# Kernel tuning notes

Hardware: AMD Instinct MI355X
Metric: run time of the kernel (lower is better)

The kernel has to match this reference:

```python
import jax, jax.numpy as jnp
import numpy as np
import math

N_EMBED = 2048
N_HEAD = 16
HEAD_DIM = N_EMBED // N_HEAD  # 128
ROPE_BASE = 10000.0


def _rope_tables(T, dim, dtype):
    # inv_freq over even indices, emb = concat(freqs, freqs) along last dim
    inv_freq = 1.0 / (ROPE_BASE ** (jnp.arange(0, dim, 2, dtype=jnp.float32) / dim))
    t = jnp.arange(T, dtype=jnp.float32)
    freqs = jnp.einsum('i,j->ij', t, inv_freq)          # [T, dim/2]
    emb = jnp.concatenate([freqs, freqs], axis=-1)      # [T, dim]
    return jnp.cos(emb).astype(dtype), jnp.sin(emb).astype(dtype)


def _rotate_half(x):
    h = x.shape[-1] // 2
    return jnp.concatenate([-x[..., h:], x[..., :h]], axis=-1)


def setup_inputs() -> dict:
    key = jax.random.key(0)
    ks = jax.random.split(key, 5)
    B, T, C = 32, 256, N_EMBED
    s = 1.0 / math.sqrt(C)
    return {
        'x': jax.random.normal(ks[0], (B, T, C), dtype=jnp.float32),
        'wq': jax.random.normal(ks[1], (C, C), dtype=jnp.float32) * s,
        'wk': jax.random.normal(ks[2], (C, C), dtype=jnp.float32) * s,
        'wv': jax.random.normal(ks[3], (C, C), dtype=jnp.float32) * s,
        'wo': jax.random.normal(ks[4], (C, C), dtype=jnp.float32) * s,
    }


def reference(x, wq, wk, wv, wo):
    B, T, C = x.shape
    H, D = N_HEAD, HEAD_DIM
    # torch Linear: y = x @ W^T
    q = (x @ wq.T).reshape(B, T, H, D).transpose(0, 2, 1, 3)  # [B,H,T,D]
    k = (x @ wk.T).reshape(B, T, H, D).transpose(0, 2, 1, 3)
    v = (x @ wv.T).reshape(B, T, H, D).transpose(0, 2, 1, 3)

    cos, sin = _rope_tables(T, D, x.dtype)  # [T,D] each, broadcast over B,H
    q = q * cos + _rotate_half(q) * sin
    k = k * cos + _rotate_half(k) * sin

    att = jnp.einsum('bhqd,bhkd->bhqk', q, k) / math.sqrt(D)
    causal = jnp.triu(jnp.ones((T, T), dtype=bool), k=1)
    att = jnp.where(causal, jnp.finfo(att.dtype).min, att)
    att = jax.nn.softmax(att, axis=-1)
    # dropout p=0.0 -> identity
    y = jnp.einsum('bhqk,bhkd->bhqd', att, v)
    y = y.transpose(0, 2, 1, 3).reshape(B, T, C)
    return y @ wo.T
```

## Files before the change

kernel.cpp:

```cpp
#include <hip/hip_runtime.h>

#define HB 32
#define HT 256
#define HC 2048
#define HH 16
#define HD 128
#define HM (HB * HT)

typedef __bf16 bf16x8 __attribute__((ext_vector_type(8)));
typedef float f32x4 __attribute__((ext_vector_type(4)));

__device__ __forceinline__ unsigned short f2bf(float f) {
  unsigned u = __float_as_uint(f);
  u += 0x7FFFu + ((u >> 16) & 1u);
  return (unsigned short)(u >> 16);
}

__global__ __launch_bounds__(256) void cvt_all(
    const float* __restrict__ x, const float* __restrict__ wq, const float* __restrict__ wk,
    const float* __restrict__ wv, const float* __restrict__ wo,
    unsigned short* __restrict__ xb, unsigned short* __restrict__ wqb,
    unsigned short* __restrict__ wkb, unsigned short* __restrict__ wvb,
    unsigned short* __restrict__ wob) {
  size_t i = (size_t)blockIdx.x * 256 + threadIdx.x;
  const float* src;
  unsigned short* dst;
  size_t off;
  if (i < 4194304) {
    src = x; dst = xb; off = i;
  } else {
    size_t j = i - 4194304;
    int w = (int)(j >> 20);
    off = j & 1048575;
    src = (w == 0) ? wq : (w == 1) ? wk : (w == 2) ? wv : wo;
    dst = (w == 0) ? wqb : (w == 1) ? wkb : (w == 2) ? wvb : wob;
  }
  float4 v = ((const float4*)src)[off];
  ushort4 o;
  o.x = f2bf(v.x); o.y = f2bf(v.y); o.z = f2bf(v.z); o.w = f2bf(v.w);
  ((ushort4*)dst)[off] = o;
}

__device__ __forceinline__ void gl_lds16(const unsigned short* g, unsigned short* l) {
  __builtin_amdgcn_global_load_lds((const __attribute__((address_space(1))) void*)g,
                                   (__attribute__((address_space(3))) void*)l, 16, 0, 0);
}

__device__ __forceinline__ void gemm_core_wide(const unsigned short* __restrict__ Ab,
                                               const unsigned short* __restrict__ Wb,
                                               unsigned short* lsA, unsigned short* lsB,
                                               f32x4 acc[4][8], int tid) {
  const int lane = tid & 63, wave = tid >> 6;
  const int l16 = lane & 15, quad = lane >> 4;
  const int wr = wave >> 1, wc = wave & 1;
  const int ch = (quad ^ ((l16 >> 1) & 3)) * 8;

  for (int kt = 0; kt < HC / 64; ++kt) {
    __syncthreads();
#pragma unroll
    for (int i = 0; i < 4; i++) {
      int c = i * 256 + tid;
      int vrow = c >> 2, slot = c & 3;
      int gc = slot ^ ((vrow >> 1) & 3);
      int row = vrow & 127, kh = vrow >> 7;
      gl_lds16(Ab + (size_t)row * HC + kt * 64 + kh * 32 + gc * 8, lsA + c * 8);
    }
#pragma unroll
    for (int i = 0; i < 8; i++) {
      int c = i * 256 + tid;
      int vrow = c >> 2, slot = c & 3;
      int gc = slot ^ ((vrow >> 1) & 3);
      int row = vrow & 255, kh = vrow >> 8;
      gl_lds16(Wb + (size_t)row * HC + kt * 64 + kh * 32 + gc * 8, lsB + c * 8);
    }
    __syncthreads();
#pragma unroll
    for (int kh = 0; kh < 2; ++kh) {
      bf16x8 af[4], bfr[8];
#pragma unroll
      for (int mi = 0; mi < 4; mi++) {
        int r = wr * 64 + mi * 16 + l16;
        af[mi] = *(const bf16x8*)(lsA + (kh * 128 + r) * 32 + ch);
      }
#pragma unroll
      for (int nj = 0; nj < 8; nj++) {
        int r = wc * 128 + nj * 16 + l16;
        bfr[nj] = *(const bf16x8*)(lsB + (kh * 256 + r) * 32 + ch);
      }
#pragma unroll
      for (int mi = 0; mi < 4; mi++)
#pragma unroll
        for (int nj = 0; nj < 8; nj++)
          acc[mi][nj] = __builtin_amdgcn_mfma_f32_16x16x32_bf16(af[mi], bfr[nj], acc[mi][nj], 0, 0, 0);
    }
  }
}

__global__ __launch_bounds__(256, 2) void gemm_out(const unsigned short* __restrict__ A,
                                                   const unsigned short* __restrict__ W,
                                                   float* __restrict__ outp) {
  __shared__ __align__(16) unsigned short lsA[2 * 128 * 32];
  __shared__ __align__(16) unsigned short lsB[2 * 256 * 32];
  const int tid = threadIdx.x;
  const int lane = tid & 63, wave = tid >> 6;
  const int l16 = lane & 15, quad = lane >> 4;
  const int wr = wave >> 1, wc = wave & 1;
  const int bm = blockIdx.x, bn = blockIdx.y;

  f32x4 acc[4][8];
#pragma unroll
  for (int i = 0; i < 4; i++)
#pragma unroll
    for (int j = 0; j < 8; j++) acc[i][j] = f32x4{0.f, 0.f, 0.f, 0.f};

  gemm_core_wide(A + (size_t)bm * 128 * HC, W + (size_t)bn * 256 * HC, lsA, lsB, acc, tid);

#pragma unroll
  for (int mi = 0; mi < 4; mi++)
#pragma unroll
    for (int nj = 0; nj < 8; nj++) {
      const int n = bn * 256 + wc * 128 + nj * 16 + l16;
#pragma unroll
      for (int rr = 0; rr < 4; rr++) {
        const int m = bm * 128 + wr * 64 + mi * 16 + quad * 4 + rr;
        outp[(size_t)m * HC + n] = acc[mi][nj][rr];
      }
    }
}

__global__ __launch_bounds__(256, 2) void gemm_qkv(const unsigned short* __restrict__ A,
                                                    const unsigned short* __restrict__ W0,
                                                    const unsigned short* __restrict__ W1,
                                                    const unsigned short* __restrict__ W2,
                                                    unsigned short* __restrict__ Qo,
                                                    unsigned short* __restrict__ Ko,
                                                    unsigned short* __restrict__ Vto) {
  __shared__ __align__(16) unsigned short lsA[2 * 128 * 32];
  __shared__ __align__(16) unsigned short lsB[2 * 256 * 32];
  const int tid = threadIdx.x;
  const int lane = tid & 63, wave = tid >> 6;
  const int l16 = lane & 15, quad = lane >> 4;
  const int wr = wave >> 1, wc = wave & 1;
  const int bm = blockIdx.x;
  const int which = blockIdx.y >> 3;
  const int bn = blockIdx.y & 7;

  f32x4 acc[4][8];
#pragma unroll
  for (int i = 0; i < 4; i++)
#pragma unroll
    for (int j = 0; j < 8; j++) acc[i][j] = f32x4{0.f, 0.f, 0.f, 0.f};

  if (which < 2) {
    const unsigned short* W = (which == 0) ? W0 : W1;
    unsigned short* outp = (which == 0) ? Qo : Ko;
    gemm_core_wide(A + (size_t)bm * 128 * HC, W + (size_t)bn * 256 * HC, lsA, lsB, acc, tid);
    const int h = bn * 2 + wc;
#pragma unroll
    for (int nj = 0; nj < 4; nj++) {
      const int dlo = nj * 16 + l16;
      const float invf = __expf((float)dlo * (-0.14391156831212787f));
#pragma unroll
      for (int mi = 0; mi < 4; mi++)
#pragma unroll
        for (int rr = 0; rr < 4; rr++) {
          const int m = bm * 128 + wr * 64 + mi * 16 + quad * 4 + rr;
          const int t = m & 255, b = m >> 8;
          float ang = (float)t * invf;
          float sn, cs;
          __sincosf(ang, &sn, &cs);
          float lo = acc[mi][nj][rr], hi = acc[mi][nj + 4][rr];
          size_t base = (((size_t)b * HH + h) * HT + t) * HD;
          outp[base + dlo] = f2bf(lo * cs - hi * sn);
          outp[base + 64 + dlo] = f2bf(hi * cs + lo * sn);
        }
    }
  } else {
    int v = bn * 64 + bm;
    int tok = v & 31, ch2 = v >> 5;
    gemm_core_wide(W2 + (size_t)ch2 * 128 * HC, A + (size_t)tok * 256 * HC, lsA, lsB, acc, tid);
    const int b = tok, h = ch2;
#pragma unroll
    for (int mi = 0; mi < 4; mi++)
#pragma unroll
      for (int nj = 0; nj < 8; nj++) {
        const int t = wc * 128 + nj * 16 + l16;
#pragma unroll
        for (int rr = 0; rr < 4; rr++) {
          const int d = wr * 64 + mi * 16 + quad * 4 + rr;
          Vto[(((size_t)b * HH + h) * HD + d) * HT + t] = f2bf(acc[mi][nj][rr]);
        }
      }
  }
}

__global__ __launch_bounds__(256) void attn_kernel(const unsigned short* __restrict__ Q,
                                                   const unsigned short* __restrict__ K,
                                                   const unsigned short* __restrict__ Vt,
                                                   unsigned short* __restrict__ Y) {
  const int g = blockIdx.x;
  const int bh = g & 511;
  const int pairp = g >> 9;
  const int wave = threadIdx.x >> 6;
  const int lane = threadIdx.x & 63;
  const int quad = lane >> 4, l16 = lane & 15;

  const unsigned short* Qh = Q + (size_t)bh * HT * HD;
  const unsigned short* Kh = K + (size_t)bh * HT * HD;
  const unsigned short* Vh = Vt + (size_t)bh * HD * HT;

  __shared__ __align__(16) unsigned short P[4][16 * 72];
  unsigned short* Pw = P[wave];

  const float scale = 0.088388347648318447f;
  const int b = bh >> 4, h = bh & 15;

  for (int half = 0; half < 2; ++half) {
    const int wq = (pairp == 0) ? (half == 0 ? 3 : 0) : (half == 0 ? 2 : 1);
    const int qrow = wq * 64 + wave * 16;

    bf16x8 qf[4];
#pragma unroll
    for (int ks = 0; ks < 4; ks++)
      qf[ks] = *(const bf16x8*)(Qh + (size_t)(qrow + l16) * HD + ks * 32 + quad * 8);

    f32x4 o[8];
#pragma unroll
    for (int di = 0; di < 8; di++) o[di] = f32x4{0.f, 0.f, 0.f, 0.f};
    float mrow[4], lrow[4];
#pragma unroll
    for (int r = 0; r < 4; r++) { mrow[r] = -1e30f; lrow[r] = 0.f; }

    for (int ct = 0; ct <= wq; ++ct) {
      f32x4 s[4];
#pragma unroll
      for (int ni = 0; ni < 4; ni++) s[ni] = f32x4{0.f, 0.f, 0.f, 0.f};
      const int nimax = (ct == wq) ? wave : 3;
#pragma unroll
      for (int ksh = 0; ksh < 2; ksh++) {
        bf16x8 kf[4][2];
#pragma unroll
        for (int ni = 0; ni < 4; ni++)
          if (ni <= nimax)
#pragma unroll
            for (int k2 = 0; k2 < 2; k2++)
              kf[ni][k2] = *(const bf16x8*)(Kh + (size_t)(ct * 64 + ni * 16 + l16) * HD +
                                            (ksh * 2 + k2) * 32 + quad * 8);
#pragma unroll
        for (int k2 = 0; k2 < 2; k2++)
#pragma unroll
          for (int ni = 0; ni < 4; ni++)
            if (ni <= nimax)
              s[ni] = __builtin_amdgcn_mfma_f32_16x16x32_bf16(qf[ksh * 2 + k2], kf[ni][k2],
                                                              s[ni], 0, 0, 0);
      }
      bf16x8 vf0[8];
#pragma unroll
      for (int di = 0; di < 8; di++)
        vf0[di] = *(const bf16x8*)(Vh + (size_t)(di * 16 + l16) * HT + ct * 64 + quad * 8);

      if (ct == wq) {
#pragma unroll
        for (int ni = 0; ni < 4; ni++)
#pragma unroll
          for (int r = 0; r < 4; r++) {
            int qr = wave * 16 + quad * 4 + r;
            int kc = ni * 16 + l16;
            s[ni][r] = (kc <= qr) ? s[ni][r] * scale : -1e30f;
          }
      } else {
#pragma unroll
        for (int ni = 0; ni < 4; ni++)
#pragma unroll
          for (int r = 0; r < 4; r++) s[ni][r] *= scale;
      }
      float pm[4];
#pragma unroll
      for (int r = 0; r < 4; r++) {
        float v = fmaxf(fmaxf(s[0][r], s[1][r]), fmaxf(s[2][r], s[3][r]));
        v = fmaxf(v, __shfl_xor(v, 1, 64));
        v = fmaxf(v, __shfl_xor(v, 2, 64));
        v = fmaxf(v, __shfl_xor(v, 4, 64));
        v = fmaxf(v, __shfl_xor(v, 8, 64));
        pm[r] = v;
      }
      float ex = fmaxf(fmaxf(pm[0] - mrow[0], pm[1] - mrow[1]),
                       fmaxf(pm[2] - mrow[2], pm[3] - mrow[3]));
      ex = fmaxf(ex, __shfl_xor(ex, 16, 64));
      ex = fmaxf(ex, __shfl_xor(ex, 32, 64));
      if (ex > 8.f) {
#pragma unroll
        for (int r = 0; r < 4; r++) {
          float mnew = fmaxf(mrow[r], pm[r]);
          float alpha = __expf(mrow[r] - mnew);
          mrow[r] = mnew;
          lrow[r] *= alpha;
#pragma unroll
          for (int di = 0; di < 8; di++) o[di][r] *= alpha;
        }
      }
#pragma unroll
      for (int r = 0; r < 4; r++) {
        float rs = 0.f;
#pragma unroll
        for (int ni = 0; ni < 4; ni++) {
          float e = __expf(s[ni][r] - mrow[r]);
          s[ni][r] = e;
          rs += e;
        }
        rs += __shfl_xor(rs, 1, 64);
        rs += __shfl_xor(rs, 2, 64);
        rs += __shfl_xor(rs, 4, 64);
        rs += __shfl_xor(rs, 8, 64);
        lrow[r] += rs;
      }
#pragma unroll
      for (int ni = 0; ni < 4; ni++)
#pragma unroll
        for (int r = 0; r < 4; r++)
          Pw[(quad * 4 + r) * 72 + ni * 16 + l16] = f2bf(s[ni][r]);
      {
        bf16x8 pf = *(const bf16x8*)(Pw + (size_t)l16 * 72 + quad * 8);
#pragma unroll
        for (int di = 0; di < 8; di++)
          o[di] = __builtin_amdgcn_mfma_f32_16x16x32_bf16(pf, vf0[di], o[di], 0, 0, 0);
      }
      {
        bf16x8 pf = *(const bf16x8*)(Pw + (size_t)l16 * 72 + 32 + quad * 8);
#pragma unroll
        for (int di = 0; di < 8; di++) {
          bf16x8 vf = *(const bf16x8*)(Vh + (size_t)(di * 16 + l16) * HT + ct * 64 + 32 + quad * 8);
          o[di] = __builtin_amdgcn_mfma_f32_16x16x32_bf16(pf, vf, o[di], 0, 0, 0);
        }
      }
    }

#pragma unroll
    for (int r = 0; r < 4; r++) {
      float inv = 1.f / lrow[r];
      int t = qrow + quad * 4 + r;
      size_t rowb = ((size_t)b * HT + t) * HC + h * HD;
#pragma unroll
      for (int di = 0; di < 8; di++)
        Y[rowb + di * 16 + l16] = f2bf(o[di][r] * inv);
    }
  }
}

extern "C" void kernel_launch(void* const* d_in, const int* in_sizes, int n_in,
                              void* d_out, int out_size, void* d_ws, size_t ws_size,
                              hipStream_t stream) {
  const float* x  = (const float*)d_in[0];
  const float* wq = (const float*)d_in[1];
  const float* wk = (const float*)d_in[2];
  const float* wv = (const float*)d_in[3];
  const float* wo = (const float*)d_in[4];
  float* out = (float*)d_out;

  char* ws = (char*)d_ws;
  const size_t MB = (size_t)1 << 20;
  unsigned short* wqb = (unsigned short*)(ws + 0 * MB);
  unsigned short* wkb = (unsigned short*)(ws + 8 * MB);
  unsigned short* wvb = (unsigned short*)(ws + 16 * MB);
  unsigned short* wob = (unsigned short*)(ws + 24 * MB);
  unsigned short* xb  = (unsigned short*)(ws + 32 * MB);
  unsigned short* Qb  = (unsigned short*)(ws + 64 * MB);
  unsigned short* Kb  = (unsigned short*)(ws + 96 * MB);
  unsigned short* Vtb = (unsigned short*)(ws + 128 * MB);
  unsigned short* Yb  = xb;

  cvt_all<<<32768, 256, 0, stream>>>(x, wq, wk, wv, wo, xb, wqb, wkb, wvb, wob);

  gemm_qkv<<<dim3(HM / 128, 24), 256, 0, stream>>>(xb, wqb, wkb, wvb, Qb, Kb, Vtb);

  attn_kernel<<<1024, 256, 0, stream>>>(Qb, Kb, Vtb, Yb);

  gemm_out<<<dim3(HM / 128, HC / 256), 256, 0, stream>>>(Yb, wob, out);
}
```

Before: 498.4 us.

## Load GEMM A fragments directly from global into registers with prefetch

```diff
diff --git a/kernel.cpp b/kernel.cpp
--- a/kernel.cpp
+++ b/kernel.cpp
@@ -46,60 +46,71 @@
                                    (__attribute__((address_space(3))) void*)l, 16, 0, 0);
 }
 
-__device__ __forceinline__ void gemm_core_wide(const unsigned short* __restrict__ Ab,
+__device__ __forceinline__ void gemm_step(const unsigned short* __restrict__ Arow,
+                                          const unsigned short* __restrict__ Wb,
+                                          unsigned short* lsB, f32x4 acc[4][8],
+                                          bf16x8 afu[2][4], bf16x8 afp[2][4],
+                                          int kt, int ktp, int tid, int ch, int wc, int l16) {
+  __syncthreads();
+#pragma unroll
+  for (int i = 0; i < 8; i++) {
+    int c = i * 256 + tid;
+    int vrow = c >> 2, slot = c & 3;
+    int gc = slot ^ ((vrow >> 1) & 3);
+    int row = vrow & 255, kh = vrow >> 8;
+    gl_lds16(Wb + (size_t)row * HC + kt * 64 + kh * 32 + gc * 8, lsB + c * 8);
+  }
+  __syncthreads();
+  if (ktp >= 0) {
+#pragma unroll
+    for (int kh = 0; kh < 2; kh++)
+#pragma unroll
+      for (int mi = 0; mi < 4; mi++)
+        afp[kh][mi] = *(const bf16x8*)(Arow + (size_t)mi * (16 * HC) + ktp * 64 + kh * 32);
+  }
+#pragma unroll
+  for (int kh = 0; kh < 2; ++kh) {
+    bf16x8 bfr[8];
+#pragma unroll
+    for (int nj = 0; nj < 8; nj++) {
+      int r = wc * 128 + nj * 16 + l16;
+      bfr[nj] = *(const bf16x8*)(lsB + (kh * 256 + r) * 32 + ch);
+    }
+#pragma unroll
+    for (int mi = 0; mi < 4; mi++)
+#pragma unroll
+      for (int nj = 0; nj < 8; nj++)
+        acc[mi][nj] = __builtin_amdgcn_mfma_f32_16x16x32_bf16(afu[kh][mi], bfr[nj], acc[mi][nj], 0, 0, 0);
+  }
+}
+
+__device__ __forceinline__ void gemm_core_wide(const unsigned short* __restrict__ Ag,
                                                const unsigned short* __restrict__ Wb,
-                                               unsigned short* lsA, unsigned short* lsB,
+                                               unsigned short* lsB,
                                                f32x4 acc[4][8], int tid) {
   const int lane = tid & 63, wave = tid >> 6;
   const int l16 = lane & 15, quad = lane >> 4;
   const int wr = wave >> 1, wc = wave & 1;
   const int ch = (quad ^ ((l16 >> 1) & 3)) * 8;
-
-  for (int kt = 0; kt < HC / 64; ++kt) {
-    __syncthreads();
-#pragma unroll
-    for (int i = 0; i < 4; i++) {
-      int c = i * 256 + tid;
-      int vrow = c >> 2, slot = c & 3;
-      int gc = slot ^ ((vrow >> 1) & 3);
-      int row = vrow & 127, kh = vrow >> 7;
-      gl_lds16(Ab + (size_t)row * HC + kt * 64 + kh * 32 + gc * 8, lsA + c * 8);
-    }
-#pragma unroll
-    for (int i = 0; i < 8; i++) {
-      int c = i * 256 + tid;
-      int vrow = c >> 2, slot = c & 3;
-      int gc = slot ^ ((vrow >> 1) & 3);
-      int row = vrow & 255, kh = vrow >> 8;
-      gl_lds16(Wb + (size_t)row * HC + kt * 64 + kh * 32 + gc * 8, lsB + c * 8);
-    }
-    __syncthreads();
-#pragma unroll
-    for (int kh = 0; kh < 2; ++kh) {
-      bf16x8 af[4], bfr[8];
-#pragma unroll
-      for (int mi = 0; mi < 4; mi++) {
-        int r = wr * 64 + mi * 16 + l16;
-        af[mi] = *(const bf16x8*)(lsA + (kh * 128 + r) * 32 + ch);
-      }
-#pragma unroll
-      for (int nj = 0; nj < 8; nj++) {
-        int r = wc * 128 + nj * 16 + l16;
-        bfr[nj] = *(const bf16x8*)(lsB + (kh * 256 + r) * 32 + ch);
-      }
-#pragma unroll
-      for (int mi = 0; mi < 4; mi++)
-#pragma unroll
-        for (int nj = 0; nj < 8; nj++)
-          acc[mi][nj] = __builtin_amdgcn_mfma_f32_16x16x32_bf16(af[mi], bfr[nj], acc[mi][nj], 0, 0, 0);
-    }
+  const unsigned short* Arow = Ag + (size_t)(wr * 64 + l16) * HC + quad * 8;
+
+  bf16x8 afA[2][4], afB[2][4];
+#pragma unroll
+  for (int kh = 0; kh < 2; kh++)
+#pragma unroll
+    for (int mi = 0; mi < 4; mi++)
+      afA[kh][mi] = *(const bf16x8*)(Arow + (size_t)mi * (16 * HC) + kh * 32);
+
+  for (int kt = 0; kt < HC / 64; kt += 2) {
+    gemm_step(Arow, Wb, lsB, acc, afA, afB, kt, kt + 1, tid, ch, wc, l16);
+    gemm_step(Arow, Wb, lsB, acc, afB, afA, kt + 1, (kt + 2 < HC / 64) ? kt + 2 : -1,
+              tid, ch, wc, l16);
   }
 }
 
 __global__ __launch_bounds__(256, 2) void gemm_out(const unsigned short* __restrict__ A,
                                                    const unsigned short* __restrict__ W,
                                                    float* __restrict__ outp) {
-  __shared__ __align__(16) unsigned short lsA[2 * 128 * 32];
   __shared__ __align__(16) unsigned short lsB[2 * 256 * 32];
   const int tid = threadIdx.x;
   const int lane = tid & 63, wave = tid >> 6;
@@ -113,7 +124,7 @@
 #pragma unroll
     for (int j = 0; j < 8; j++) acc[i][j] = f32x4{0.f, 0.f, 0.f, 0.f};
 
-  gemm_core_wide(A + (size_t)bm * 128 * HC, W + (size_t)bn * 256 * HC, lsA, lsB, acc, tid);
+  gemm_core_wide(A + (size_t)bm * 128 * HC, W + (size_t)bn * 256 * HC, lsB, acc, tid);
 
 #pragma unroll
   for (int mi = 0; mi < 4; mi++)
@@ -135,7 +146,6 @@
                                                     unsigned short* __restrict__ Qo,
                                                     unsigned short* __restrict__ Ko,
                                                     unsigned short* __restrict__ Vto) {
-  __shared__ __align__(16) unsigned short lsA[2 * 128 * 32];
   __shared__ __align__(16) unsigned short lsB[2 * 256 * 32];
   const int tid = threadIdx.x;
   const int lane = tid & 63, wave = tid >> 6;
@@ -154,7 +164,7 @@
   if (which < 2) {
     const unsigned short* W = (which == 0) ? W0 : W1;
     unsigned short* outp = (which == 0) ? Qo : Ko;
-    gemm_core_wide(A + (size_t)bm * 128 * HC, W + (size_t)bn * 256 * HC, lsA, lsB, acc, tid);
+    gemm_core_wide(A + (size_t)bm * 128 * HC, W + (size_t)bn * 256 * HC, lsB, acc, tid);
     const int h = bn * 2 + wc;
 #pragma unroll
     for (int nj = 0; nj < 4; nj++) {
@@ -178,7 +188,7 @@
   } else {
     int v = bn * 64 + bm;
     int tok = v & 31, ch2 = v >> 5;
-    gemm_core_wide(W2 + (size_t)ch2 * 128 * HC, A + (size_t)tok * 256 * HC, lsA, lsB, acc, tid);
+    gemm_core_wide(W2 + (size_t)ch2 * 128 * HC, A + (size_t)tok * 256 * HC, lsB, acc, tid);
     const int b = tok, h = ch2;
 #pragma unroll
     for (int mi = 0; mi < 4; mi++)
```

New measurement: 903.7 us. 81.3% more time.
